# Kernel optimization log

Hardware: AMD Instinct MI355X
Metric: run time of the kernel (lower is better)

## Reference

```python
import jax, jax.numpy as jnp
import numpy as np

B, T, Q, K = 64, 2048, 512, 512

def setup_inputs() -> dict:
    key0 = jax.random.key(0)
    k1, k2, k3 = jax.random.split(key0, 3)
    query = jax.random.normal(k1, (B, Q), dtype=jnp.float32)
    key = jax.random.normal(k2, (B, T, K), dtype=jnp.float32)
    # learned params: weights ~ U(-0.1, 0.1), bias zeros(1)
    W = jax.random.uniform(k3, (K, Q), dtype=jnp.float32) * 0.2 - 0.1
    bias = jnp.zeros((1,), dtype=jnp.float32)
    return {"query": query, "key": key, "W": W, "bias": bias}

def reference(query, key, W, bias):
    # mids = W @ query : [B, K]
    mids = jnp.einsum('kq,bq->bk', W, query)
    # scores = tanh(key . mids + bias) : [B, T]
    scores = jnp.tanh(jnp.einsum('btk,bk->bt', key, mids) + bias)
    return jax.nn.softmax(scores, axis=1)
```

## Files before the change

kernel.cpp:

```cpp
#include <hip/hip_runtime.h>
#include <math.h>

#define WAVE 64

typedef float nfloat4 __attribute__((ext_vector_type(4)));


__global__ void mids_kernel(const float* __restrict__ W,
                            const float* __restrict__ query,
                            float* __restrict__ mids) {
    const int gwave = (int)((blockIdx.x * blockDim.x + threadIdx.x) >> 6);
    const int lane  = threadIdx.x & 63;
    const int b  = gwave >> 6;
    const int k0 = (gwave & 63) * 8;

    const float4* qrow = (const float4*)(query + (size_t)b * 512);
    const float4 q0 = qrow[lane];
    const float4 q1 = qrow[lane + 64];

    float s[8];
    #pragma unroll
    for (int r = 0; r < 8; ++r) {
        const float4* wrow = (const float4*)(W + (size_t)(k0 + r) * 512);
        float4 a = wrow[lane];
        float4 c = wrow[lane + 64];
        s[r] = a.x*q0.x + a.y*q0.y + a.z*q0.z + a.w*q0.w
             + c.x*q1.x + c.y*q1.y + c.z*q1.z + c.w*q1.w;
    }
    #pragma unroll
    for (int off = 32; off > 0; off >>= 1) {
        #pragma unroll
        for (int r = 0; r < 8; ++r)
            s[r] += __shfl_xor(s[r], off, WAVE);
    }
    if (lane == 0) {
        float4* dst = (float4*)(mids + (size_t)gwave * 8);
        dst[0] = make_float4(s[0], s[1], s[2], s[3]);
        dst[1] = make_float4(s[4], s[5], s[6], s[7]);
    }
}

__global__ void scores_kernel(const float* __restrict__ key,
                              const float* __restrict__ mids,
                              const float* __restrict__ bias,
                              float* __restrict__ out) {
    const int gwave = (int)((blockIdx.x * blockDim.x + threadIdx.x) >> 6);
    const int lane  = threadIdx.x & 63;
    const int row0  = gwave * 16;
    const int b     = row0 >> 11;

    const float4* mrow = (const float4*)(mids + (size_t)b * 512);
    const float4 m0 = mrow[lane];
    const float4 m1 = mrow[lane + 64];
    const float bv = bias[0];

    const nfloat4* kbase = (const nfloat4*)key + (size_t)row0 * 128;

    #pragma unroll
    for (int g = 0; g < 2; ++g) {
        const int r0 = g * 8;
        nfloat4 a[8], c[8];
        #pragma unroll
        for (int r = 0; r < 8; ++r) {
            a[r] = __builtin_nontemporal_load(&kbase[(size_t)(r0 + r) * 128 + lane]);
            c[r] = __builtin_nontemporal_load(&kbase[(size_t)(r0 + r) * 128 + lane + 64]);
        }
        float s[8];
        #pragma unroll
        for (int r = 0; r < 8; ++r) {
            s[r] = a[r].x*m0.x + a[r].y*m0.y + a[r].z*m0.z + a[r].w*m0.w
                 + c[r].x*m1.x + c[r].y*m1.y + c[r].z*m1.z + c[r].w*m1.w;
        }
        #pragma unroll
        for (int off = 32; off > 0; off >>= 1) {
            #pragma unroll
            for (int r = 0; r < 8; ++r)
                s[r] += __shfl_xor(s[r], off, WAVE);
        }
        if (lane == 0) {
            *(float4*)(out + (size_t)row0 + r0) =
                make_float4(tanhf(s[0] + bv), tanhf(s[1] + bv),
                            tanhf(s[2] + bv), tanhf(s[3] + bv));
            *(float4*)(out + (size_t)row0 + r0 + 4) =
                make_float4(tanhf(s[4] + bv), tanhf(s[5] + bv),
                            tanhf(s[6] + bv), tanhf(s[7] + bv));
        }
    }
}

__global__ void softmax_kernel(float* __restrict__ out, int T) {
    const int b    = blockIdx.x;
    const int tid  = threadIdx.x;
    const int lane = tid & (WAVE - 1);
    const int wid  = tid >> 6;
    float* row = out + (size_t)b * T;

    __shared__ float red[4];

    float vals[8];
    float m = -INFINITY;
    #pragma unroll
    for (int i = 0; i < 8; ++i) {
        vals[i] = row[tid + i * 256];
        m = fmaxf(m, vals[i]);
    }
    #pragma unroll
    for (int off = 32; off > 0; off >>= 1)
        m = fmaxf(m, __shfl_xor(m, off, WAVE));
    if (lane == 0) red[wid] = m;
    __syncthreads();
    m = fmaxf(fmaxf(red[0], red[1]), fmaxf(red[2], red[3]));
    __syncthreads();

    float s = 0.f;
    #pragma unroll
    for (int i = 0; i < 8; ++i) {
        vals[i] = expf(vals[i] - m);
        s += vals[i];
    }
    #pragma unroll
    for (int off = 32; off > 0; off >>= 1)
        s += __shfl_xor(s, off, WAVE);
    if (lane == 0) red[wid] = s;
    __syncthreads();
    s = red[0] + red[1] + red[2] + red[3];

    float inv = 1.f / s;
    #pragma unroll
    for (int i = 0; i < 8; ++i)
        row[tid + i * 256] = vals[i] * inv;
}

extern "C" void kernel_launch(void* const* d_in, const int* in_sizes, int n_in,
                              void* d_out, int out_size, void* d_ws, size_t ws_size,
                              hipStream_t stream) {
    const float* query = (const float*)d_in[0];
    const float* key   = (const float*)d_in[1];
    const float* W     = (const float*)d_in[2];
    const float* bias  = (const float*)d_in[3];
    float* out  = (float*)d_out;
    float* mids = (float*)d_ws;

    const int B = 64, T = 2048;

    mids_kernel<<<1024, 256, 0, stream>>>(W, query, mids);

    scores_kernel<<<2048, 256, 0, stream>>>(key, mids, bias, out);

    softmax_kernel<<<B, 256, 0, stream>>>(out, T);
}
```

Before: 346.8 us.

## Fuse exp and row sums into scores kernel, use transpose-style reduction

Replaces the 8-way butterfly shuffle reduction with a transpose-style reduce8 that halves the number of values at each step, cutting shuffle count. The scores kernel now computes exp(tanh(x+b)) directly, skipping max subtraction because tanh bounds the input to [-1,1]. Per-batch sums are accumulated with atomics into a workspace buffer zeroed in the mids kernel. The old softmax is replaced by a simple elementwise normalize kernel with more blocks. Summation order is no longer deterministic because of the float atomics.

```diff
diff --git a/kernel.cpp b/kernel.cpp
--- a/kernel.cpp
+++ b/kernel.cpp
@@ -6,9 +6,40 @@
 typedef float nfloat4 __attribute__((ext_vector_type(4)));
 
 
+__device__ __forceinline__ float reduce8(const float s[8]) {
+    const int lane = (int)(threadIdx.x & 63);
+    const bool hi32 = (lane & 32) != 0;
+    float v[4];
+    #pragma unroll
+    for (int r = 0; r < 4; ++r) {
+        float keep = hi32 ? s[r + 4] : s[r];
+        float send = hi32 ? s[r] : s[r + 4];
+        v[r] = keep + __shfl_xor(send, 32, WAVE);
+    }
+    const bool hi16 = (lane & 16) != 0;
+    float w[2];
+    #pragma unroll
+    for (int r = 0; r < 2; ++r) {
+        float keep = hi16 ? v[r + 2] : v[r];
+        float send = hi16 ? v[r] : v[r + 2];
+        w[r] = keep + __shfl_xor(send, 16, WAVE);
+    }
+    const bool hi8 = (lane & 8) != 0;
+    float keep = hi8 ? w[1] : w[0];
+    float send = hi8 ? w[0] : w[1];
+    float x = keep + __shfl_xor(send, 8, WAVE);
+    x += __shfl_xor(x, 4, WAVE);
+    x += __shfl_xor(x, 2, WAVE);
+    x += __shfl_xor(x, 1, WAVE);
+    return x;
+}
+
 __global__ void mids_kernel(const float* __restrict__ W,
                             const float* __restrict__ query,
-                            float* __restrict__ mids) {
+                            float* __restrict__ mids,
+                            float* __restrict__ sums) {
+    if (blockIdx.x == 0 && threadIdx.x < 64) sums[threadIdx.x] = 0.f;
+
     const int gwave = (int)((blockIdx.x * blockDim.x + threadIdx.x) >> 6);
     const int lane  = threadIdx.x & 63;
     const int b  = gwave >> 6;
@@ -27,23 +58,16 @@
         s[r] = a.x*q0.x + a.y*q0.y + a.z*q0.z + a.w*q0.w
              + c.x*q1.x + c.y*q1.y + c.z*q1.z + c.w*q1.w;
     }
-    #pragma unroll
-    for (int off = 32; off > 0; off >>= 1) {
-        #pragma unroll
-        for (int r = 0; r < 8; ++r)
-            s[r] += __shfl_xor(s[r], off, WAVE);
-    }
-    if (lane == 0) {
-        float4* dst = (float4*)(mids + (size_t)gwave * 8);
-        dst[0] = make_float4(s[0], s[1], s[2], s[3]);
-        dst[1] = make_float4(s[4], s[5], s[6], s[7]);
-    }
+    float x = reduce8(s);
+    if ((lane & 7) == 0)
+        mids[(size_t)gwave * 8 + ((lane >> 3) & 7)] = x;
 }
 
 __global__ void scores_kernel(const float* __restrict__ key,
                               const float* __restrict__ mids,
                               const float* __restrict__ bias,
-                              float* __restrict__ out) {
+                              float* __restrict__ out,
+                              float* __restrict__ sums) {
     const int gwave = (int)((blockIdx.x * blockDim.x + threadIdx.x) >> 6);
     const int lane  = threadIdx.x & 63;
     const int row0  = gwave * 16;
@@ -55,6 +79,8 @@
     const float bv = bias[0];
 
     const nfloat4* kbase = (const nfloat4*)key + (size_t)row0 * 128;
+
+    float wave_sum = 0.f;
 
     #pragma unroll
     for (int g = 0; g < 2; ++g) {
@@ -71,64 +97,29 @@
             s[r] = a[r].x*m0.x + a[r].y*m0.y + a[r].z*m0.z + a[r].w*m0.w
                  + c[r].x*m1.x + c[r].y*m1.y + c[r].z*m1.z + c[r].w*m1.w;
         }
-        #pragma unroll
-        for (int off = 32; off > 0; off >>= 1) {
-            #pragma unroll
-            for (int r = 0; r < 8; ++r)
-                s[r] += __shfl_xor(s[r], off, WAVE);
-        }
-        if (lane == 0) {
-            *(float4*)(out + (size_t)row0 + r0) =
-                make_float4(tanhf(s[0] + bv), tanhf(s[1] + bv),
-                            tanhf(s[2] + bv), tanhf(s[3] + bv));
-            *(float4*)(out + (size_t)row0 + r0 + 4) =
-                make_float4(tanhf(s[4] + bv), tanhf(s[5] + bv),
-                            tanhf(s[6] + bv), tanhf(s[7] + bv));
-        }
+        float x = reduce8(s);
+        float e = expf(tanhf(x + bv));
+        if ((lane & 7) == 0)
+            out[(size_t)row0 + r0 + ((lane >> 3) & 7)] = e;
+        float y = e;
+        y += __shfl_xor(y, 8, WAVE);
+        y += __shfl_xor(y, 16, WAVE);
+        y += __shfl_xor(y, 32, WAVE);
+        wave_sum += y;
     }
+    if (lane == 0)
+        atomicAdd(&sums[b], wave_sum);
 }
 
-__global__ void softmax_kernel(float* __restrict__ out, int T) {
-    const int b    = blockIdx.x;
-    const int tid  = threadIdx.x;
-    const int lane = tid & (WAVE - 1);
-    const int wid  = tid >> 6;
-    float* row = out + (size_t)b * T;
-
-    __shared__ float red[4];
-
-    float vals[8];
-    float m = -INFINITY;
-    #pragma unroll
-    for (int i = 0; i < 8; ++i) {
-        vals[i] = row[tid + i * 256];
-        m = fmaxf(m, vals[i]);
-    }
-    #pragma unroll
-    for (int off = 32; off > 0; off >>= 1)
-        m = fmaxf(m, __shfl_xor(m, off, WAVE));
-    if (lane == 0) red[wid] = m;
-    __syncthreads();
-    m = fmaxf(fmaxf(red[0], red[1]), fmaxf(red[2], red[3]));
-    __syncthreads();
-
-    float s = 0.f;
-    #pragma unroll
-    for (int i = 0; i < 8; ++i) {
-        vals[i] = expf(vals[i] - m);
-        s += vals[i];
-    }
-    #pragma unroll
-    for (int off = 32; off > 0; off >>= 1)
-        s += __shfl_xor(s, off, WAVE);
-    if (lane == 0) red[wid] = s;
-    __syncthreads();
-    s = red[0] + red[1] + red[2] + red[3];
-
-    float inv = 1.f / s;
-    #pragma unroll
-    for (int i = 0; i < 8; ++i)
-        row[tid + i * 256] = vals[i] * inv;
+__global__ void normalize_kernel(float* __restrict__ out,
+                                 const float* __restrict__ sums) {
+    const int idx = (int)(blockIdx.x * blockDim.x + threadIdx.x);
+    const int b   = idx >> 9;
+    const float inv = 1.f / sums[b];
+    float4* p = (float4*)out + idx;
+    float4 v = *p;
+    v.x *= inv; v.y *= inv; v.z *= inv; v.w *= inv;
+    *p = v;
 }
 
 extern "C" void kernel_launch(void* const* d_in, const int* in_sizes, int n_in,
@@ -140,12 +131,11 @@
     const float* bias  = (const float*)d_in[3];
     float* out  = (float*)d_out;
     float* mids = (float*)d_ws;
+    float* sums = mids + 64 * 512;
 
-    const int B = 64, T = 2048;
+    mids_kernel<<<1024, 256, 0, stream>>>(W, query, mids, sums);
 
-    mids_kernel<<<1024, 256, 0, stream>>>(W, query, mids);
+    scores_kernel<<<2048, 256, 0, stream>>>(key, mids, bias, out, sums);
 
-    scores_kernel<<<2048, 256, 0, stream>>>(key, mids, bias, out);
-
-    softmax_kernel<<<B, 256, 0, stream>>>(out, T);
+    normalize_kernel<<<128, 256, 0, stream>>>(out, sums);
 }
```

Result: slower. 382.8 us (+10.4%).
